# Optimization experiments

Measured on AMD Instinct MI355X. Metric: run time of the kernel, lower is better.

The kernel has to match this reference:

```python
import jax, jax.numpy as jnp
import numpy as np

N_NODES = 100000


def gcn_conv(x, W, b, src, dst, n_nodes):
    # PyG GCNConv: h = x @ W; add self-loops; sym-normalized scatter-add; + bias
    loop = jnp.arange(n_nodes, dtype=src.dtype)
    src2 = jnp.concatenate([src, loop])
    dst2 = jnp.concatenate([dst, loop])
    deg = jax.ops.segment_sum(jnp.ones(src2.shape, x.dtype), dst2, num_segments=n_nodes)
    dinv = jax.lax.rsqrt(deg)  # deg >= 1 thanks to self-loops
    norm = dinv[src2] * dinv[dst2]                 # [E+N]
    h = x @ W                                      # [N, out]
    msg = h[src2] * norm[:, None]                  # gather + scale, [E+N, out]
    out = jax.ops.segment_sum(msg, dst2, num_segments=n_nodes)  # scatter-add
    return out + b


def setup_inputs() -> dict:
    key = jax.random.key(0)
    k1, k2, k3, k4, k5 = jax.random.split(key, 5)
    nfeat, nhid = 128, 64
    n_edges = 1600000
    x = jax.random.normal(k1, (N_NODES, nfeat), dtype=jnp.float32)
    edge_index = jax.random.randint(k2, (2, n_edges), 0, N_NODES, dtype=jnp.int64)
    W1 = jax.random.normal(k3, (nfeat, nhid), dtype=jnp.float32) / np.sqrt(nfeat)
    b1 = jnp.zeros((nhid,), jnp.float32)
    W2 = jax.random.normal(k4, (nhid, nhid), dtype=jnp.float32) / np.sqrt(nhid)
    b2 = jnp.zeros((nhid,), jnp.float32)
    return {"x": x, "edge_index": edge_index, "W1": W1, "b1": b1, "W2": W2, "b2": b2}


def reference(x, edge_index, W1, b1, W2, b2):
    # eval mode: dropout is identity
    src, dst = edge_index[0], edge_index[1]
    h = jax.nn.relu(gcn_conv(x, W1, b1, src, dst, N_NODES))
    residual = h
    out = jax.nn.relu(gcn_conv(h, W2, b2, src, dst, N_NODES))
    return out + residual
```

## Files before the change

### kernel.cpp

```cpp
#include <hip/hip_runtime.h>

#define N_NODES 100000
#define NDUMMY 100000
#define NH 64
#define NB 500
#define NPB 200
#define BCAP 4096
#define PBCAP 6400
#define EPB 8192


__device__ __forceinline__ unsigned short f2bf(float f) {
    union { float f; unsigned int i; } c;
    c.f = f;
    unsigned int b = c.i;
    b += 0x7FFFu + ((b >> 16) & 1u);
    return (unsigned short)(b >> 16);
}

__device__ __forceinline__ unsigned pack2bf(float lo, float hi) {
    return (unsigned)f2bf(lo) | ((unsigned)f2bf(hi) << 16);
}

__device__ __forceinline__ float bfLO(unsigned u) {
    union { unsigned i; float f; } c; c.i = u << 16; return c.f;
}
__device__ __forceinline__ float bfHI(unsigned u) {
    union { unsigned i; float f; } c; c.i = u & 0xFFFF0000u; return c.f;
}


__global__ __launch_bounds__(512) void k_init(int* __restrict__ bcur, unsigned* __restrict__ dummy_row) {
    int t = threadIdx.x;
    if (t < NB) bcur[t] = 0;
    if (t < 32) dummy_row[t] = 0;
}


__global__ __launch_bounds__(1024) void k_sort(const int* __restrict__ src, const int* __restrict__ dst,
                                               int* __restrict__ bcur, unsigned* __restrict__ ebuf, int e) {
    __shared__ unsigned sorted[EPB];
    __shared__ unsigned short cellof[EPB];
    __shared__ int lh[512];
    __shared__ int lbase[512];
    __shared__ int lcur[512];
    __shared__ int gpos[512];
    __shared__ int wsum[8];
    const int t = threadIdx.x;
    const int e0 = blockIdx.x * EPB;
    int cnt = e - e0; if (cnt > EPB) cnt = EPB;

    if (t < 512) lh[t] = 0;
    __syncthreads();

    for (int i = t * 4; i < cnt; i += 4096) {
        int4 d4 = *(const int4*)&dst[e0 + i];
        atomicAdd(&lh[d4.x / NPB], 1);
        atomicAdd(&lh[d4.y / NPB], 1);
        atomicAdd(&lh[d4.z / NPB], 1);
        atomicAdd(&lh[d4.w / NPB], 1);
    }
    __syncthreads();

    const int lane = t & 63, wave = t >> 6;
    int v = 0, inc = 0;
    if (t < 512) {
        v = (t < NB) ? lh[t] : 0;
        inc = v;
#pragma unroll
        for (int d = 1; d < 64; d <<= 1) {
            int u = __shfl_up(inc, d, 64);
            if (lane >= d) inc += u;
        }
        if (lane == 63) wsum[wave] = inc;
    }
    __syncthreads();
    if (t < NB) {
        int woff = 0;
#pragma unroll
        for (int w = 0; w < 8; ++w)
            if (w < wave) woff += wsum[w];
        const int excl = woff + inc - v;
        lbase[t] = excl;
        lcur[t] = excl;
        gpos[t] = atomicAdd(&bcur[t], v);
    }
    __syncthreads();

    for (int i = t * 4; i < cnt; i += 4096) {
        int4 d4 = *(const int4*)&dst[e0 + i];
        int4 s4 = *(const int4*)&src[e0 + i];
        int b0 = d4.x / NPB, b1 = d4.y / NPB, b2 = d4.z / NPB, b3 = d4.w / NPB;
        int p0 = atomicAdd(&lcur[b0], 1);
        int p1 = atomicAdd(&lcur[b1], 1);
        int p2 = atomicAdd(&lcur[b2], 1);
        int p3 = atomicAdd(&lcur[b3], 1);
        sorted[p0] = ((unsigned)(d4.x - b0 * NPB) << 17) | (unsigned)s4.x; cellof[p0] = (unsigned short)b0;
        sorted[p1] = ((unsigned)(d4.y - b1 * NPB) << 17) | (unsigned)s4.y; cellof[p1] = (unsigned short)b1;
        sorted[p2] = ((unsigned)(d4.z - b2 * NPB) << 17) | (unsigned)s4.z; cellof[p2] = (unsigned short)b2;
        sorted[p3] = ((unsigned)(d4.w - b3 * NPB) << 17) | (unsigned)s4.w; cellof[p3] = (unsigned short)b3;
    }
    __syncthreads();

    for (int i = t * 4; i < cnt; i += 4096) {
        uint4 sv = *(const uint4*)&sorted[i];
        ushort4 cv = *(const ushort4*)&cellof[i];
        int c0 = cv.x, c1 = cv.y, c2 = cv.z, c3 = cv.w;
        int g0 = gpos[c0] + (i + 0 - lbase[c0]);
        int g1 = gpos[c1] + (i + 1 - lbase[c1]);
        int g2 = gpos[c2] + (i + 2 - lbase[c2]);
        int g3 = gpos[c3] + (i + 3 - lbase[c3]);
        if (g0 < BCAP) ebuf[(long long)c0 * BCAP + g0] = sv.x;
        if (g1 < BCAP) ebuf[(long long)c1 * BCAP + g1] = sv.y;
        if (g2 < BCAP) ebuf[(long long)c2 * BCAP + g2] = sv.z;
        if (g3 < BCAP) ebuf[(long long)c3 * BCAP + g3] = sv.w;
    }
}

__global__ __launch_bounds__(256) void k_build(const unsigned* __restrict__ ebuf, const int* __restrict__ bcur,
                                               int* __restrict__ rowptr, int* __restrict__ degp,
                                               float* __restrict__ dinv, int* __restrict__ csrc, int n) {
    __shared__ unsigned ls[BCAP];
    __shared__ int lh[256];
    __shared__ int lpv[256];
    __shared__ int lstart[256];
    __shared__ int lc[256];
    __shared__ int wsum[4];
    const int b = blockIdx.x;
    const int t = threadIdx.x;
    const int node0 = b * NPB;
    int count = bcur[b];
    if (count > BCAP) count = BCAP;
    const int rbase = b * PBCAP;

    lh[t] = 0;
    for (int i = t; i < count; i += 256) ls[i] = ebuf[(long long)b * BCAP + i];
    __syncthreads();
    for (int i = t; i < count; i += 256) atomicAdd(&lh[ls[i] >> 17], 1);
    __syncthreads();

    const int v = lh[t];
    lpv[t] = (v + 7) & ~7;
    __syncthreads();
    const int g = t & ~7;
    int pvg = lpv[g];
#pragma unroll
    for (int j = 1; j < 8; ++j) pvg = max(pvg, lpv[g + j]);

    const int lane = t & 63, wave = t >> 6;
    int inc = pvg;
#pragma unroll
    for (int d = 1; d < 64; d <<= 1) {
        int u = __shfl_up(inc, d, 64);
        if (lane >= d) inc += u;
    }
    if (lane == 63) wsum[wave] = inc;
    __syncthreads();
    int woff = 0;
#pragma unroll
    for (int w = 0; w < 4; ++w)
        if (w < wave) woff += wsum[w];
    const int start = rbase + woff + inc - pvg;

    lstart[t] = start;
    lc[t] = start;
    const int node = node0 + t;
    if (t < NPB && node < n) {
        rowptr[node] = start;
        degp[node] = pvg;
        dinv[node] = rsqrtf((float)(v + 1));
    }
    __syncthreads();

    for (int i = t; i < count; i += 256) {
        unsigned u = ls[i];
        int pos = atomicAdd(&lc[u >> 17], 1);
        csrc[pos] = (int)(u & 0x1FFFFu);
    }
    __syncthreads();

    const int pend = lstart[t] + pvg;
    for (int p = lc[t]; p < pend; ++p) csrc[p] = NDUMMY;
}


typedef __attribute__((ext_vector_type(8))) short bf16x8;
typedef __attribute__((ext_vector_type(4))) float f32x4;

template <int K>
__global__ __launch_bounds__(256) void k_gemm_mfma(const float* __restrict__ X, const float* __restrict__ W,
                                                   const float* __restrict__ dinv,
                                                   unsigned short* __restrict__ out, int n) {
    constexpr int KP = K + 8;
    constexpr int KH = K / 2;
    constexpr int WP = (K == 128) ? 68 : 40;
    constexpr int NKS = K / 32;
    __shared__ unsigned short xs[128][KP];
    __shared__ unsigned wsb[64][WP];
    const int tid = threadIdx.x;
    const int lane = tid & 63;
    const int wv = tid >> 6;
    const int n0 = blockIdx.x * 128;
    const int col = lane & 15;
    const int q = lane >> 4;
    const int krow = q * 8;

    for (int idx = tid * 4; idx < 128 * K; idx += 1024) {
        int row = idx / K, c = idx % K;
        float4 v = make_float4(0.f, 0.f, 0.f, 0.f);
        if (n0 + row < n) v = *(const float4*)&X[(long long)(n0 + row) * K + c];
        ushort4 o;
        o.x = f2bf(v.x); o.y = f2bf(v.y); o.z = f2bf(v.z); o.w = f2bf(v.w);
        *(ushort4*)&xs[row][c] = o;
    }

    for (int idx = tid; idx < 64 * KH; idx += 256) {
        int c = idx & 63, k2 = idx >> 6;
        float w0 = W[(2 * k2) * NH + c];
        float w1 = W[(2 * k2 + 1) * NH + c];
        wsb[c][k2] = pack2bf(w0, w1);
    }
    __syncthreads();

    f32x4 zero = {0.f, 0.f, 0.f, 0.f};
    f32x4 acc[2][4];
#pragma unroll
    for (int mt = 0; mt < 2; ++mt)
#pragma unroll
        for (int nt = 0; nt < 4; ++nt) acc[mt][nt] = zero;

#pragma unroll
    for (int ks = 0; ks < NKS; ++ks) {
        bf16x8 b[4];
#pragma unroll
        for (int nt = 0; nt < 4; ++nt)
            b[nt] = *(const bf16x8*)&wsb[nt * 16 + col][ks * 16 + q * 4];
#pragma unroll
        for (int mt = 0; mt < 2; ++mt) {
            const int r = wv * 32 + mt * 16 + col;
            bf16x8 a = *(const bf16x8*)&xs[r][ks * 32 + krow];
#pragma unroll
            for (int nt = 0; nt < 4; ++nt)
                acc[mt][nt] = __builtin_amdgcn_mfma_f32_16x16x32_bf16(a, b[nt], acc[mt][nt], 0, 0, 0);
        }
    }

#pragma unroll
    for (int mt = 0; mt < 2; ++mt) {
#pragma unroll
        for (int r = 0; r < 4; ++r) {
            int node = n0 + wv * 32 + mt * 16 + q * 4 + r;
            if (node < n) {
                float dv = dinv[node];
#pragma unroll
                for (int nt = 0; nt < 4; ++nt)
                    out[(long long)node * NH + nt * 16 + col] = f2bf(acc[mt][nt][r] * dv);
            }
        }
    }
}


__global__ __launch_bounds__(256) void k_agg(const unsigned* __restrict__ hs32, const float* __restrict__ dinv,
                                             const int* __restrict__ rowptr, const int* __restrict__ degp,
                                             const int* __restrict__ csrc,
                                             const float* __restrict__ bias, const float* __restrict__ resid,
                                             float* __restrict__ out, int n) {
    const int gt = blockIdx.x * 256 + threadIdx.x;
    const int wave = gt >> 6;
    const int lane = threadIdx.x & 63;
    const int sub = lane >> 3;
    const int li = lane & 7;
    const int node = wave * 8 + sub;
    if (node >= n) return;

    const uint4* hsv = (const uint4*)hs32;
    uint4 su = hsv[node * 8 + li];
    float a0 = bfLO(su.x), a1 = bfHI(su.x), a2 = bfLO(su.y), a3 = bfHI(su.y);
    float a4 = bfLO(su.z), a5 = bfHI(su.z), a6 = bfLO(su.w), a7 = bfHI(su.w);
    float b0 = 0.f, b1 = 0.f, b2 = 0.f, b3 = 0.f, b4 = 0.f, b5 = 0.f, b6 = 0.f, b7 = 0.f;

    const int rp = rowptr[node];
    const int dg = degp[node];
    int4 c0, c1;
    if (dg > 0) {
        c0 = *(const int4*)&csrc[rp];
        c1 = *(const int4*)&csrc[rp + 4];
    }
    for (int e = 0; e < dg; e += 8) {
        const int4 m0 = c0, m1 = c1;
        if (e + 8 < dg) {
            c0 = *(const int4*)&csrc[rp + e + 8];
            c1 = *(const int4*)&csrc[rp + e + 12];
        }
        uint4 u0 = hsv[m0.x * 8 + li];
        uint4 u1 = hsv[m0.y * 8 + li];
        uint4 u2 = hsv[m0.z * 8 + li];
        uint4 u3 = hsv[m0.w * 8 + li];
        uint4 u4 = hsv[m1.x * 8 + li];
        uint4 u5 = hsv[m1.y * 8 + li];
        uint4 u6 = hsv[m1.z * 8 + li];
        uint4 u7 = hsv[m1.w * 8 + li];
        a0 += bfLO(u0.x); a1 += bfHI(u0.x); a2 += bfLO(u0.y); a3 += bfHI(u0.y);
        a4 += bfLO(u0.z); a5 += bfHI(u0.z); a6 += bfLO(u0.w); a7 += bfHI(u0.w);
        b0 += bfLO(u1.x); b1 += bfHI(u1.x); b2 += bfLO(u1.y); b3 += bfHI(u1.y);
        b4 += bfLO(u1.z); b5 += bfHI(u1.z); b6 += bfLO(u1.w); b7 += bfHI(u1.w);
        a0 += bfLO(u2.x); a1 += bfHI(u2.x); a2 += bfLO(u2.y); a3 += bfHI(u2.y);
        a4 += bfLO(u2.z); a5 += bfHI(u2.z); a6 += bfLO(u2.w); a7 += bfHI(u2.w);
        b0 += bfLO(u3.x); b1 += bfHI(u3.x); b2 += bfLO(u3.y); b3 += bfHI(u3.y);
        b4 += bfLO(u3.z); b5 += bfHI(u3.z); b6 += bfLO(u3.w); b7 += bfHI(u3.w);
        a0 += bfLO(u4.x); a1 += bfHI(u4.x); a2 += bfLO(u4.y); a3 += bfHI(u4.y);
        a4 += bfLO(u4.z); a5 += bfHI(u4.z); a6 += bfLO(u4.w); a7 += bfHI(u4.w);
        b0 += bfLO(u5.x); b1 += bfHI(u5.x); b2 += bfLO(u5.y); b3 += bfHI(u5.y);
        b4 += bfLO(u5.z); b5 += bfHI(u5.z); b6 += bfLO(u5.w); b7 += bfHI(u5.w);
        a0 += bfLO(u6.x); a1 += bfHI(u6.x); a2 += bfLO(u6.y); a3 += bfHI(u6.y);
        a4 += bfLO(u6.z); a5 += bfHI(u6.z); a6 += bfLO(u6.w); a7 += bfHI(u6.w);
        b0 += bfLO(u7.x); b1 += bfHI(u7.x); b2 += bfLO(u7.y); b3 += bfHI(u7.y);
        b4 += bfLO(u7.z); b5 += bfHI(u7.z); b6 += bfLO(u7.w); b7 += bfHI(u7.w);
    }
    const float dv = dinv[node];
    const float4 ba = *(const float4*)&bias[8 * li];
    const float4 bb = *(const float4*)&bias[8 * li + 4];
    float v0 = fmaxf(dv * (a0 + b0) + ba.x, 0.f);
    float v1 = fmaxf(dv * (a1 + b1) + ba.y, 0.f);
    float v2 = fmaxf(dv * (a2 + b2) + ba.z, 0.f);
    float v3 = fmaxf(dv * (a3 + b3) + ba.w, 0.f);
    float v4 = fmaxf(dv * (a4 + b4) + bb.x, 0.f);
    float v5 = fmaxf(dv * (a5 + b5) + bb.y, 0.f);
    float v6 = fmaxf(dv * (a6 + b6) + bb.z, 0.f);
    float v7 = fmaxf(dv * (a7 + b7) + bb.w, 0.f);
    const long long ob = (long long)node * NH + 8 * li;
    if (resid) {
        float4 r0 = *(const float4*)&resid[ob];
        float4 r1 = *(const float4*)&resid[ob + 4];
        v0 += r0.x; v1 += r0.y; v2 += r0.z; v3 += r0.w;
        v4 += r1.x; v5 += r1.y; v6 += r1.z; v7 += r1.w;
    }
    *(float4*)&out[ob] = make_float4(v0, v1, v2, v3);
    *(float4*)&out[ob + 4] = make_float4(v4, v5, v6, v7);
}


extern "C" void kernel_launch(void* const* d_in, const int* in_sizes, int n_in,
                              void* d_out, int out_size, void* d_ws, size_t ws_size,
                              hipStream_t stream) {
    const float* x  = (const float*)d_in[0];
    const int*   ei = (const int*)d_in[1];
    const float* W1 = (const float*)d_in[2];
    const float* b1 = (const float*)d_in[3];
    const float* W2 = (const float*)d_in[4];
    const float* b2 = (const float*)d_in[5];
    float* out = (float*)d_out;

    const int N = N_NODES;
    const int E = in_sizes[1] / 2;
    const int* src = ei;
    const int* dst = ei + E;

    const int NP = 100352;
    int*   bcur   = (int*)d_ws;
    int*   rowptr = bcur + 512;
    int*   degp   = rowptr + NP;
    float* dinv   = (float*)(degp + NP);
    int*   csrc   = (int*)(dinv + NP);
    unsigned* ebuf = (unsigned*)(csrc + NB * PBCAP);
    unsigned* hs32 = ebuf;
    unsigned short* hsb = (unsigned short*)hs32;
    float* h1     = (float*)(hs32 + (long long)(NDUMMY + 1) * 32);

    const int nb_sort = (E + EPB - 1) / EPB;

    k_init<<<1, 512, 0, stream>>>(bcur, hs32 + (long long)NDUMMY * 32);
    k_sort<<<nb_sort, 1024, 0, stream>>>(src, dst, bcur, ebuf, E);
    k_build<<<NB, 256, 0, stream>>>(ebuf, bcur, rowptr, degp, dinv, csrc, N);

    k_gemm_mfma<128><<<(N + 127) / 128, 256, 0, stream>>>(x, W1, dinv, hsb, N);
    k_agg<<<(N + 31) / 32, 256, 0, stream>>>(hs32, dinv, rowptr, degp, csrc, b1, nullptr, h1, N);

    k_gemm_mfma<64><<<(N + 127) / 128, 256, 0, stream>>>(h1, W2, dinv, hsb, N);
    k_agg<<<(N + 31) / 32, 256, 0, stream>>>(hs32, dinv, rowptr, degp, csrc, b2, h1, out, N);
}
```

Measured before the change: 137.0 us.

## Load GEMM A-fragments directly from global into registers, drop LDS staging

The MFMA GEMM no longer stages the converted X tile in shared memory. Each lane loads its own MFMA A-fragment straight from global memory as float4 pairs, converts it to bf16 in registers, and feeds the MFMA directly. The block tile shrinks from 128 to 64 rows, so twice as many blocks launch, and the W tile is still built in LDS. This removes an LDS write/read round trip and cuts LDS use, which may raise occupancy. The cost is less-coalesced strided global loads and W being repacked by twice as many blocks.

```diff
diff --git a/kernel.cpp b/kernel.cpp
--- a/kernel.cpp
+++ b/kernel.cpp
@@ -191,71 +191,67 @@
 __global__ __launch_bounds__(256) void k_gemm_mfma(const float* __restrict__ X, const float* __restrict__ W,
                                                    const float* __restrict__ dinv,
                                                    unsigned short* __restrict__ out, int n) {
-    constexpr int KP = K + 8;
     constexpr int KH = K / 2;
     constexpr int WP = (K == 128) ? 68 : 40;
     constexpr int NKS = K / 32;
-    __shared__ unsigned short xs[128][KP];
     __shared__ unsigned wsb[64][WP];
     const int tid = threadIdx.x;
     const int lane = tid & 63;
     const int wv = tid >> 6;
-    const int n0 = blockIdx.x * 128;
+    const int n0 = blockIdx.x * 64;
     const int col = lane & 15;
     const int q = lane >> 4;
-    const int krow = q * 8;
-
-    for (int idx = tid * 4; idx < 128 * K; idx += 1024) {
-        int row = idx / K, c = idx % K;
-        float4 v = make_float4(0.f, 0.f, 0.f, 0.f);
-        if (n0 + row < n) v = *(const float4*)&X[(long long)(n0 + row) * K + c];
-        ushort4 o;
-        o.x = f2bf(v.x); o.y = f2bf(v.y); o.z = f2bf(v.z); o.w = f2bf(v.w);
-        *(ushort4*)&xs[row][c] = o;
+
+    const int row = n0 + wv * 16 + col;
+    const int rc = (row < n) ? row : (n - 1);
+    const float* xp = X + (long long)rc * K + q * 8;
+    float4 xa[NKS], xb[NKS];
+#pragma unroll
+    for (int ks = 0; ks < NKS; ++ks) {
+        xa[ks] = *(const float4*)&xp[ks * 32];
+        xb[ks] = *(const float4*)&xp[ks * 32 + 4];
     }
 
     for (int idx = tid; idx < 64 * KH; idx += 256) {
         int c = idx & 63, k2 = idx >> 6;
-        float w0 = W[(2 * k2) * NH + c];
-        float w1 = W[(2 * k2 + 1) * NH + c];
-        wsb[c][k2] = pack2bf(w0, w1);
+        wsb[c][k2] = pack2bf(W[(2 * k2) * NH + c], W[(2 * k2 + 1) * NH + c]);
+    }
+
+    union FragU { bf16x8 v; unsigned u[4]; };
+    bf16x8 afrag[NKS];
+#pragma unroll
+    for (int ks = 0; ks < NKS; ++ks) {
+        FragU f;
+        f.u[0] = pack2bf(xa[ks].x, xa[ks].y);
+        f.u[1] = pack2bf(xa[ks].z, xa[ks].w);
+        f.u[2] = pack2bf(xb[ks].x, xb[ks].y);
+        f.u[3] = pack2bf(xb[ks].z, xb[ks].w);
+        afrag[ks] = f.v;
     }
     __syncthreads();
 
     f32x4 zero = {0.f, 0.f, 0.f, 0.f};
-    f32x4 acc[2][4];
-#pragma unroll
-    for (int mt = 0; mt < 2; ++mt)
-#pragma unroll
-        for (int nt = 0; nt < 4; ++nt) acc[mt][nt] = zero;
+    f32x4 acc[4];
+#pragma unroll
+    for (int nt = 0; nt < 4; ++nt) acc[nt] = zero;
 
 #pragma unroll
     for (int ks = 0; ks < NKS; ++ks) {
-        bf16x8 b[4];
-#pragma unroll
-        for (int nt = 0; nt < 4; ++nt)
-            b[nt] = *(const bf16x8*)&wsb[nt * 16 + col][ks * 16 + q * 4];
-#pragma unroll
-        for (int mt = 0; mt < 2; ++mt) {
-            const int r = wv * 32 + mt * 16 + col;
-            bf16x8 a = *(const bf16x8*)&xs[r][ks * 32 + krow];
+#pragma unroll
+        for (int nt = 0; nt < 4; ++nt) {
+            bf16x8 b = *(const bf16x8*)&wsb[nt * 16 + col][ks * 16 + q * 4];
+            acc[nt] = __builtin_amdgcn_mfma_f32_16x16x32_bf16(afrag[ks], b, acc[nt], 0, 0, 0);
+        }
+    }
+
+#pragma unroll
+    for (int r = 0; r < 4; ++r) {
+        int node = n0 + wv * 16 + q * 4 + r;
+        if (node < n) {
+            float dv = dinv[node];
 #pragma unroll
             for (int nt = 0; nt < 4; ++nt)
-                acc[mt][nt] = __builtin_amdgcn_mfma_f32_16x16x32_bf16(a, b[nt], acc[mt][nt], 0, 0, 0);
-        }
-    }
-
-#pragma unroll
-    for (int mt = 0; mt < 2; ++mt) {
-#pragma unroll
-        for (int r = 0; r < 4; ++r) {
-            int node = n0 + wv * 32 + mt * 16 + q * 4 + r;
-            if (node < n) {
-                float dv = dinv[node];
-#pragma unroll
-                for (int nt = 0; nt < 4; ++nt)
-                    out[(long long)node * NH + nt * 16 + col] = f2bf(acc[mt][nt][r] * dv);
-            }
+                out[(long long)node * NH + nt * 16 + col] = f2bf(acc[nt][r] * dv);
         }
     }
 }
@@ -374,9 +370,9 @@
     k_sort<<<nb_sort, 1024, 0, stream>>>(src, dst, bcur, ebuf, E);
     k_build<<<NB, 256, 0, stream>>>(ebuf, bcur, rowptr, degp, dinv, csrc, N);
 
-    k_gemm_mfma<128><<<(N + 127) / 128, 256, 0, stream>>>(x, W1, dinv, hsb, N);
+    k_gemm_mfma<128><<<(N + 63) / 64, 256, 0, stream>>>(x, W1, dinv, hsb, N);
     k_agg<<<(N + 31) / 32, 256, 0, stream>>>(hs32, dinv, rowptr, degp, csrc, b1, nullptr, h1, N);
 
-    k_gemm_mfma<64><<<(N + 127) / 128, 256, 0, stream>>>(h1, W2, dinv, hsb, N);
+    k_gemm_mfma<64><<<(N + 63) / 64, 256, 0, stream>>>(h1, W2, dinv, hsb, N);
     k_agg<<<(N + 31) / 32, 256, 0, stream>>>(hs32, dinv, rowptr, degp, csrc, b2, h1, out, N);
 }
```

Result: faster. 131.3 us (-4.2%).
